# Kernel tuning notes

Hardware: AMD Instinct MI355X
Metric: run time of the kernel (lower is better)

Reference implementation:

```python
import jax, jax.numpy as jnp
import numpy as np

B, C = 8192, 128


def setup_inputs() -> dict:
    key = jax.random.key(0)
    k1, k2 = jax.random.split(key)
    mu_in = jax.random.normal(k1, (B, C), dtype=jnp.float32)
    Sigma_in = jax.random.normal(k2, (B, C, C), dtype=jnp.float32)
    return {"mu_in": mu_in, "Sigma_in": Sigma_in}


def reference(mu_in, Sigma_in):
    # softmax over the class dim
    mu_out = jax.nn.softmax(mu_in, axis=-1)            # [B, C]
    # Jacobian of softmax: diag(p) - p p^T             # [B, C, C]
    ppT = mu_out[:, :, None] * mu_out[:, None, :]
    grad = jnp.zeros_like(ppT).at[:, jnp.arange(C), jnp.arange(C)].set(mu_out) - ppT
    # Sigma_out = J Sigma J^T via two batched matmuls
    Sigma_out = jnp.einsum('bij,bjk,blk->bil', grad, Sigma_in, grad)
    return (mu_out, Sigma_out)
```

## Files before the change

kernel.cpp:

```cpp
#include <hip/hip_runtime.h>
#include <math.h>


#define C 128
#define STRIDE 129
#define BLOCK 256
#define F4_PER_TILE (C * C / 4)

__device__ __forceinline__ float wave_reduce_sum(float v) {
    #pragma unroll
    for (int off = 32; off > 0; off >>= 1) v += __shfl_xor(v, off, 64);
    return v;
}
__device__ __forceinline__ float wave_reduce_max(float v) {
    #pragma unroll
    for (int off = 32; off > 0; off >>= 1) v = fmaxf(v, __shfl_xor(v, off, 64));
    return v;
}

__global__ __launch_bounds__(BLOCK, 1) void jsj_kernel(
    const float* __restrict__ mu_in,
    const float* __restrict__ Sigma_in,
    float* __restrict__ mu_out,
    float* __restrict__ Sigma_out)
{
    const int b    = blockIdx.x;
    const int t    = threadIdx.x;
    const int wave = t >> 6;
    const int lane = t & 63;

    __shared__ float S[C * STRIDE];
    __shared__ float p[C];
    __shared__ float rs[C];
    __shared__ float ss[C];
    __shared__ float red[8];

    const float4* Sg = (const float4*)(Sigma_in + (size_t)b * (C * C));
    float4 v[16];
    #pragma unroll
    for (int it = 0; it < 16; ++it)
        v[it] = Sg[t + it * BLOCK];

    float x = (t < C) ? mu_in[b * C + t] : -INFINITY;
    float m = wave_reduce_max(x);
    if (lane == 0) red[wave] = m;
    __syncthreads();
    m = fmaxf(fmaxf(red[0], red[1]), fmaxf(red[2], red[3]));
    float e = (t < C) ? expf(x - m) : 0.0f;
    float es = wave_reduce_sum(e);
    if (lane == 0) red[4 + wave] = es;
    __syncthreads();
    float denom = red[4] + red[5] + red[6] + red[7];
    float pt = e / denom;
    if (t < C) { p[t] = pt; mu_out[b * C + t] = pt; }

    #pragma unroll
    for (int it = 0; it < 16; ++it) {
        int f   = t + it * BLOCK;
        int row = f >> 5;
        int col = (f & 31) << 2;
        float* dst = &S[row * STRIDE + col];
        dst[0] = v[it].x; dst[1] = v[it].y; dst[2] = v[it].z; dst[3] = v[it].w;
    }
    __syncthreads();

    float acc = 0.0f;
    if (t < C) {
        const float* row = &S[t * STRIDE];
        #pragma unroll 8
        for (int k = 0; k < C; ++k) acc += row[k] * p[k];
        rs[t] = acc;
    } else {
        const int l = t - C;
        #pragma unroll 8
        for (int j = 0; j < C; ++j) acc += p[j] * S[j * STRIDE + l];
        ss[l] = acc;
    }
    __syncthreads();

    float val = (t < C) ? rs[t] * p[t] : 0.0f;
    float wq = wave_reduce_sum(val);
    if (lane == 0) red[wave] = wq;
    __syncthreads();
    const float q = red[0] + red[1] + red[2] + red[3];

    float4* Og = (float4*)(Sigma_out + (size_t)b * (C * C));
    #pragma unroll
    for (int it = 0; it < 16; ++it) {
        int f    = t + it * BLOCK;
        int row  = f >> 5;
        int col  = (f & 31) << 2;
        float pi   = p[row];
        float base = q - rs[row];
        const float* srow = &S[row * STRIDE + col];
        float4 o;
        o.x = pi * p[col + 0] * (srow[0] - ss[col + 0] + base);
        o.y = pi * p[col + 1] * (srow[1] - ss[col + 1] + base);
        o.z = pi * p[col + 2] * (srow[2] - ss[col + 2] + base);
        o.w = pi * p[col + 3] * (srow[3] - ss[col + 3] + base);
        Og[f] = o;
    }
}

extern "C" void kernel_launch(void* const* d_in, const int* in_sizes, int n_in,
                              void* d_out, int out_size, void* d_ws, size_t ws_size,
                              hipStream_t stream) {
    const float* mu_in    = (const float*)d_in[0];
    const float* Sigma_in = (const float*)d_in[1];
    const int B = in_sizes[0] / C;

    float* mu_out    = (float*)d_out;
    float* Sigma_out = (float*)d_out + (size_t)B * C;

    jsj_kernel<<<B, BLOCK, 0, stream>>>(mu_in, Sigma_in, mu_out, Sigma_out);
}
```

Baseline: 862.1 us.

## Keep Sigma tile in registers and compute row/column sums via shuffles

Removes the 64KB shared-memory staging of each 128x128 Sigma tile. Row sums (Sigma p) are now computed with 32-lane shuffle reductions, column sums (p^T Sigma) as per-thread float4 partials combined through a small shared array, and the output is produced straight from the register-held tile. With far less LDS per block and launch bounds raised to 4 blocks per CU, more blocks can be resident per CU to hide HBM latency. The risks are extra shuffle work and register pressure from holding 16 float4 values per thread.

```diff
diff --git a/kernel.cpp b/kernel.cpp
--- a/kernel.cpp
+++ b/kernel.cpp
@@ -3,10 +3,13 @@
 
 
 #define C 128
-#define STRIDE 129
 #define BLOCK 256
-#define F4_PER_TILE (C * C / 4)
 
+__device__ __forceinline__ float reduce32_sum(float v) {
+    #pragma unroll
+    for (int off = 16; off > 0; off >>= 1) v += __shfl_xor(v, off, 64);
+    return v;
+}
 __device__ __forceinline__ float wave_reduce_sum(float v) {
     #pragma unroll
     for (int off = 32; off > 0; off >>= 1) v += __shfl_xor(v, off, 64);
@@ -18,7 +21,7 @@
     return v;
 }
 
-__global__ __launch_bounds__(BLOCK, 1) void jsj_kernel(
+__global__ __launch_bounds__(BLOCK, 4) void jsj_kernel(
     const float* __restrict__ mu_in,
     const float* __restrict__ Sigma_in,
     float* __restrict__ mu_out,
@@ -28,12 +31,13 @@
     const int t    = threadIdx.x;
     const int wave = t >> 6;
     const int lane = t & 63;
+    const int g    = t >> 5;
+    const int cq   = t & 31;
 
-    __shared__ float S[C * STRIDE];
-    __shared__ float p[C];
-    __shared__ float rs[C];
-    __shared__ float ss[C];
-    __shared__ float red[8];
+    __shared__ float  p[C];
+    __shared__ float  rs[C];
+    __shared__ float  red[8];
+    __shared__ float4 sp[8][32];
 
     const float4* Sg = (const float4*)(Sigma_in + (size_t)b * (C * C));
     float4 v[16];
@@ -53,52 +57,51 @@
     float denom = red[4] + red[5] + red[6] + red[7];
     float pt = e / denom;
     if (t < C) { p[t] = pt; mu_out[b * C + t] = pt; }
+    __syncthreads();
 
+    const float4 p4 = *(const float4*)&p[cq * 4];
+
+    float4 s4 = make_float4(0.f, 0.f, 0.f, 0.f);
+    float qpart = 0.0f;
     #pragma unroll
     for (int it = 0; it < 16; ++it) {
-        int f   = t + it * BLOCK;
-        int row = f >> 5;
-        int col = (f & 31) << 2;
-        float* dst = &S[row * STRIDE + col];
-        dst[0] = v[it].x; dst[1] = v[it].y; dst[2] = v[it].z; dst[3] = v[it].w;
+        const int row  = g + 8 * it;
+        const float pr = p[row];
+        float part = v[it].x * p4.x + v[it].y * p4.y
+                   + v[it].z * p4.z + v[it].w * p4.w;
+        qpart += pr * part;
+        s4.x  += pr * v[it].x;
+        s4.y  += pr * v[it].y;
+        s4.z  += pr * v[it].z;
+        s4.w  += pr * v[it].w;
+        float r = reduce32_sum(part);
+        if (cq == 0) rs[row] = r;
     }
+    sp[g][cq] = s4;
+    qpart = wave_reduce_sum(qpart);
+    if (lane == 0) red[wave] = qpart;
     __syncthreads();
 
-    float acc = 0.0f;
-    if (t < C) {
-        const float* row = &S[t * STRIDE];
-        #pragma unroll 8
-        for (int k = 0; k < C; ++k) acc += row[k] * p[k];
-        rs[t] = acc;
-    } else {
-        const int l = t - C;
-        #pragma unroll 8
-        for (int j = 0; j < C; ++j) acc += p[j] * S[j * STRIDE + l];
-        ss[l] = acc;
+    const float q = red[0] + red[1] + red[2] + red[3];
+    float4 ss4 = sp[0][cq];
+    #pragma unroll
+    for (int gg = 1; gg < 8; ++gg) {
+        float4 w = sp[gg][cq];
+        ss4.x += w.x; ss4.y += w.y; ss4.z += w.z; ss4.w += w.w;
     }
-    __syncthreads();
-
-    float val = (t < C) ? rs[t] * p[t] : 0.0f;
-    float wq = wave_reduce_sum(val);
-    if (lane == 0) red[wave] = wq;
-    __syncthreads();
-    const float q = red[0] + red[1] + red[2] + red[3];
 
     float4* Og = (float4*)(Sigma_out + (size_t)b * (C * C));
     #pragma unroll
     for (int it = 0; it < 16; ++it) {
-        int f    = t + it * BLOCK;
-        int row  = f >> 5;
-        int col  = (f & 31) << 2;
-        float pi   = p[row];
-        float base = q - rs[row];
-        const float* srow = &S[row * STRIDE + col];
+        const int row   = g + 8 * it;
+        const float pi  = p[row];
+        const float base = q - rs[row];
         float4 o;
-        o.x = pi * p[col + 0] * (srow[0] - ss[col + 0] + base);
-        o.y = pi * p[col + 1] * (srow[1] - ss[col + 1] + base);
-        o.z = pi * p[col + 2] * (srow[2] - ss[col + 2] + base);
-        o.w = pi * p[col + 3] * (srow[3] - ss[col + 3] + base);
-        Og[f] = o;
+        o.x = pi * p4.x * (v[it].x - ss4.x + base);
+        o.y = pi * p4.y * (v[it].y - ss4.y + base);
+        o.z = pi * p4.z * (v[it].z - ss4.z + base);
+        o.w = pi * p4.w * (v[it].w - ss4.w + base);
+        Og[t + it * BLOCK] = o;
     }
 }
 
```

After: 859.0 us. About the same (-0.4%).
